# Performance work log

Hardware: AMD Instinct MI355X
Metric: run time of the kernel (lower is better)

The kernel has to match this reference:

```python
import jax, jax.numpy as jnp
import numpy as np

HEADS = 20          # 1280 / 64 head_dim, standard SD UNet attention
LORA_SCALE = 1.0    # lora_scale init arg


def setup_inputs() -> dict:
    key = jax.random.key(0)
    ks = jax.random.split(key, 16)
    def w(k, shape, s=0.02):
        return jax.random.normal(k, shape, dtype=jnp.float32) * s
    H, C, R = 1280, 768, 64  # hidden_size, cross_attention_dim, lora_rank
    return {
        "hidden_states": jax.random.normal(ks[0], (16, 4096, H), dtype=jnp.float32),
        "encoder_hidden_states": jax.random.normal(ks[1], (16, 77, C), dtype=jnp.float32),
        # base attention projections (diffusers: q/k/v no bias, to_out has bias)
        "Wq": w(ks[2], (H, H)), "Wk": w(ks[3], (C, H)), "Wv": w(ks[4], (C, H)),
        "Wo": w(ks[5], (H, H)), "bo": jnp.zeros((H,), dtype=jnp.float32),
        # LoRA adapters (down: in->rank, up: rank->out, no bias)
        "q_down": w(ks[6], (H, R)), "q_up": w(ks[7], (R, H)),
        "k_down": w(ks[8], (C, R)), "k_up": w(ks[9], (R, H)),
        "v_down": w(ks[10], (C, R)), "v_up": w(ks[11], (R, H)),
        "o_down": w(ks[12], (H, R)), "o_up": w(ks[13], (R, H)),
    }


def reference(hidden_states, encoder_hidden_states, Wq, Wk, Wv, Wo, bo,
              q_down, q_up, k_down, k_up, v_down, v_up, o_down, o_up):
    b, sq, _ = hidden_states.shape
    # base projections + LoRA low-rank corrections
    q = hidden_states @ Wq + LORA_SCALE * ((hidden_states @ q_down) @ q_up)
    k = encoder_hidden_states @ Wk + LORA_SCALE * ((encoder_hidden_states @ k_down) @ k_up)
    v = encoder_hidden_states @ Wv + LORA_SCALE * ((encoder_hidden_states @ v_down) @ v_up)

    d = q.shape[-1] // HEADS
    def split_heads(x):  # [b, s, h*d] -> [b, h, s, d]
        return x.reshape(x.shape[0], x.shape[1], HEADS, d).transpose(0, 2, 1, 3)
    qh, kh, vh = split_heads(q), split_heads(k), split_heads(v)

    # scaled dot-product attention (no mask, non-causal, dropout=0)
    scale = 1.0 / np.sqrt(d).astype(np.float32)
    scores = jnp.einsum('bhqd,bhkd->bhqk', qh, kh) * scale
    probs = jax.nn.softmax(scores, axis=-1)
    attn_out = jnp.einsum('bhqk,bhkd->bhqd', probs, vh)
    attn_out = attn_out.transpose(0, 2, 1, 3).reshape(b, sq, HEADS * d)

    # output projection + LoRA on W_O
    out = attn_out @ Wo + bo + LORA_SCALE * ((attn_out @ o_down) @ o_up)
    return out
```

## Files before the change

### kernel.cpp

```cpp
#include <hip/hip_runtime.h>
#include <hip/hip_bf16.h>
#include <stdint.h>

typedef unsigned short u16;
typedef __attribute__((ext_vector_type(8))) short short8;
typedef __attribute__((ext_vector_type(4))) float f32x4;

__device__ __forceinline__ u16 f2bf(float f) {
  union { float f; unsigned u; } v; v.f = f;
  unsigned r = v.u + 0x7fffu + ((v.u >> 16) & 1u);
  return (u16)(r >> 16);
}

__device__ __forceinline__ void g2lds16(const u16* g, u16* l) {
  __builtin_amdgcn_global_load_lds(
      (const __attribute__((address_space(1))) uint32_t*)g,
      (__attribute__((address_space(3))) uint32_t*)l, 16, 0, 0);
}

#define BAR()   asm volatile("s_barrier" ::: "memory")
#define LGKM0() asm volatile("s_waitcnt lgkmcnt(0)" ::: "memory")
#define VM8()   asm volatile("s_waitcnt vmcnt(8)" ::: "memory")
#define VM0()   asm volatile("s_waitcnt vmcnt(0)" ::: "memory")
#define PRIO1() __builtin_amdgcn_s_setprio(1)
#define PRIO0() __builtin_amdgcn_s_setprio(0)

#define QSCALE 0.18033688f

__global__ __launch_bounds__(256) void k_convert(const float* __restrict__ in,
                                                 u16* __restrict__ out, int n8) {
  int i = blockIdx.x * 256 + threadIdx.x;
  if (i >= n8) return;
  const float4* p = (const float4*)(in + (size_t)i * 8);
  float4 a = p[0], b = p[1];
  short8 o;
  o[0] = (short)f2bf(a.x); o[1] = (short)f2bf(a.y);
  o[2] = (short)f2bf(a.z); o[3] = (short)f2bf(a.w);
  o[4] = (short)f2bf(b.x); o[5] = (short)f2bf(b.y);
  o[6] = (short)f2bf(b.z); o[7] = (short)f2bf(b.w);
  *(short8*)(out + (size_t)i * 8) = o;
}

__global__ __launch_bounds__(256) void k_convert_pad(const float* __restrict__ in,
                                                     u16* __restrict__ out,
                                                     int n8_valid, int n8_total) {
  int i = blockIdx.x * 256 + threadIdx.x;
  if (i >= n8_total) return;
  short8 o;
  if (i < n8_valid) {
    const float4* p = (const float4*)(in + (size_t)i * 8);
    float4 a = p[0], b = p[1];
    o[0] = (short)f2bf(a.x); o[1] = (short)f2bf(a.y);
    o[2] = (short)f2bf(a.z); o[3] = (short)f2bf(a.w);
    o[4] = (short)f2bf(b.x); o[5] = (short)f2bf(b.y);
    o[6] = (short)f2bf(b.z); o[7] = (short)f2bf(b.w);
  } else {
#pragma unroll
    for (int e = 0; e < 8; ++e) o[e] = 0;
  }
  *(short8*)(out + (size_t)i * 8) = o;
}

__global__ __launch_bounds__(256) void k_fusew(const float* __restrict__ W,
                                               const float* __restrict__ dn_g,
                                               const float* __restrict__ up_g,
                                               u16* __restrict__ Wt, int K, int N) {
  __shared__ float dn[64][65];
  __shared__ float up[64][17];
  const int k0 = blockIdx.x * 64, n0 = blockIdx.y * 16;
  const int kc = threadIdx.x & 63, ty = threadIdx.x >> 6;
  for (int c = threadIdx.x; c < 4096; c += 256)
    dn[c >> 6][c & 63] = dn_g[(size_t)(k0 + (c >> 6)) * 64 + (c & 63)];
  for (int c = threadIdx.x; c < 1024; c += 256)
    up[c >> 4][c & 15] = up_g[(size_t)(c >> 4) * N + n0 + (c & 15)];
  __syncthreads();
  float acc[4];
#pragma unroll
  for (int e = 0; e < 4; ++e)
    acc[e] = W[(size_t)(k0 + kc) * N + n0 + ty * 4 + e];
#pragma unroll 16
  for (int r = 0; r < 64; ++r) {
    float d = dn[kc][r];
#pragma unroll
    for (int e = 0; e < 4; ++e) acc[e] += d * up[r][ty * 4 + e];
  }
#pragma unroll
  for (int e = 0; e < 4; ++e)
    Wt[(size_t)(n0 + ty * 4 + e) * K + k0 + kc] = f2bf(acc[e]);
}

template <int OUT_MODE>
__global__ __launch_bounds__(256) void k_gemm(const u16* __restrict__ A,
                                              const u16* __restrict__ Bt,
                                              void* __restrict__ Cout,
                                              const float* __restrict__ bias,
                                              int M, int N, int K) {
  __shared__ __align__(16) u16 As[128 * 32];
  __shared__ __align__(16) u16 Bs[128 * 32];
  const int tid = threadIdx.x, lane = tid & 63, w = tid >> 6;
  const int n0 = blockIdx.x * 128, m0 = blockIdx.y * 128;
  const int wm = (w >> 1) * 64, wn = (w & 1) * 64;

  f32x4 acc[4][4];
  f32x4 zf = {0.f, 0.f, 0.f, 0.f};
#pragma unroll
  for (int i = 0; i < 4; ++i)
#pragma unroll
    for (int j = 0; j < 4; ++j) acc[i][j] = zf;

  const int c0 = w, c1 = w + 4;
  const int rA0 = c0 * 16 + (lane >> 2), rA1 = c1 * 16 + (lane >> 2);
  const int kp = (lane & 3) * 8;
  const u16* gA0 = A + (size_t)(m0 + rA0) * K + kp;
  const u16* gA1 = A + (size_t)(m0 + rA1) * K + kp;
  const u16* gB0 = Bt + (size_t)(n0 + rA0) * K + kp;
  const u16* gB1 = Bt + (size_t)(n0 + rA1) * K + kp;
  u16* lA0 = As + c0 * 512;  u16* lA1 = As + c1 * 512;
  u16* lB0 = Bs + c0 * 512;  u16* lB1 = Bs + c1 * 512;

  const int fr = lane & 15, kg = (lane >> 4) * 8;

  for (int k0 = 0; k0 < K; k0 += 32) {
    g2lds16(gA0 + k0, lA0);
    g2lds16(gA1 + k0, lA1);
    g2lds16(gB0 + k0, lB0);
    g2lds16(gB1 + k0, lB1);
    __syncthreads();
    short8 af[4], bf[4];
#pragma unroll
    for (int i = 0; i < 4; ++i)
      af[i] = *(const short8*)(As + (wm + i * 16 + fr) * 32 + kg);
#pragma unroll
    for (int j = 0; j < 4; ++j)
      bf[j] = *(const short8*)(Bs + (wn + j * 16 + fr) * 32 + kg);
#pragma unroll
    for (int i = 0; i < 4; ++i)
#pragma unroll
      for (int j = 0; j < 4; ++j)
        acc[i][j] = __builtin_amdgcn_mfma_f32_16x16x32_bf16(af[i], bf[j], acc[i][j], 0, 0, 0);
    __syncthreads();
  }

  const int rb = (lane >> 4) * 4;
  if (OUT_MODE == 0) {
    u16* C = (u16*)Cout;
#pragma unroll
    for (int i = 0; i < 4; ++i)
#pragma unroll
      for (int j = 0; j < 4; ++j) {
        int col = n0 + wn + j * 16 + fr;
#pragma unroll
        for (int r = 0; r < 4; ++r) {
          int row = m0 + wm + i * 16 + rb + r;
          C[(size_t)row * N + col] = f2bf(acc[i][j][r]);
        }
      }
  } else {
    float* C = (float*)Cout;
#pragma unroll
    for (int i = 0; i < 4; ++i)
#pragma unroll
      for (int j = 0; j < 4; ++j) {
        int col = n0 + wn + j * 16 + fr;
        float bj = bias[col];
#pragma unroll
        for (int r = 0; r < 4; ++r) {
          int row = m0 + wm + i * 16 + rb + r;
          C[(size_t)row * N + col] = acc[i][j][r] + bj;
        }
      }
  }
}


#define GEMM256_TILE_RD()                                                      \
  constexpr int K = 1280;                                                      \
  constexpr int N = 1280;                                                      \
  __shared__ __align__(16) u16 lds[2][2][2][128 * 64];                         \
  const int lane = threadIdx.x & 63, w = threadIdx.x >> 6;                     \
  const int bid = blockIdx.x;                                                  \
  const int tile = (bid & 7) * 160 + (bid >> 3);                               \
  const int n0 = (tile % 5) * 256, m0 = (tile / 5) * 256;                      \
  const int l0 = w * 2;                                                        \
  const int fr = lane & 15;                                                    \
  const int q16b = (lane >> 4) * 16;                                           \
  const int xr = (fr & 7) << 4;                                                \
  const int cT0 = ((0 + q16b) ^ xr) >> 1;                                      \
  const int cT1 = ((64 + q16b) ^ xr) >> 1;                                     \
  const int ha = w >> 2;                                                       \
  const int hb = (w & 3) >> 1;                                                 \
  const int rB0 = (w & 1) * 64;

#define LOAD_AF(P, IB)                                                         \
  do {                                                                         \
    _Pragma("unroll") for (int ii = 0; ii < 4; ++ii) {                         \
      const u16* rp = &lds[P][0][ha][(((IB) + ii) * 16 + fr) * 64];            \
      af[ii][0] = *(const short8*)(rp + cT0);                                  \
      af[ii][1] = *(const short8*)(rp + cT1);                                  \
    }                                                                          \
  } while (0)

#define LOAD_BF(P, JB)                                                         \
  do {                                                                         \
    _Pragma("unroll") for (int jj = 0; jj < 2; ++jj) {                         \
      const u16* rp = &lds[P][1][hb][(rB0 + ((JB) + jj) * 16 + fr) * 64];      \
      bf[(JB) + jj][0] = *(const short8*)(rp + cT0);                           \
      bf[(JB) + jj][1] = *(const short8*)(rp + cT1);                           \
    }                                                                          \
  } while (0)

#define MFMA_Q(IO, JB)                                                         \
  do {                                                                         \
    _Pragma("unroll") for (int t = 0; t < 2; ++t)                              \
        _Pragma("unroll") for (int ii = 0; ii < 4; ++ii)                       \
            _Pragma("unroll") for (int jj = 0; jj < 2; ++jj)                   \
                acc[(IO) + ii][(JB) + jj] =                                    \
        __builtin_amdgcn_mfma_f32_16x16x32_bf16(                               \
            af[ii][t], bf[(JB) + jj][t], acc[(IO) + ii][(JB) + jj], 0, 0, 0);  \
  } while (0)

#define ACC_ZERO()                                                             \
  do {                                                                         \
    f32x4 zf = {0.f, 0.f, 0.f, 0.f};                                           \
    _Pragma("unroll") for (int i = 0; i < 8; ++i)                              \
        _Pragma("unroll") for (int j = 0; j < 4; ++j) acc[i][j] = zf;          \
  } while (0)

template <int OUT_MODE>
__global__ __launch_bounds__(512, 2) void k_gemm256f(const u16* __restrict__ A,
                                                     const u16* __restrict__ Bt,
                                                     void* __restrict__ Cout,
                                                     const float* __restrict__ bias) {
  GEMM256_TILE_RD();
  const u16* gsrc[8];
#pragma unroll
  for (int s = 0; s < 8; ++s) {
    const int side = s >> 2, h = (s >> 1) & 1, l = s & 1;
    const int o = (l0 + l) * 1024 + lane * 16;
    const int row = o >> 7;
    const int scol = (o & 127) ^ ((row & 7) << 4);
    const u16* base = side ? (Bt + (size_t)(n0 + h * 128 + row) * K)
                           : (A + (size_t)(m0 + h * 128 + row) * K);
    gsrc[s] = base + (scol >> 1);
  }

#define STAGE(P, KT)                                                           \
  do {                                                                         \
    _Pragma("unroll") for (int s = 0; s < 8; ++s) {                            \
      const int side = s >> 2, h = (s >> 1) & 1, l = s & 1;                    \
      g2lds16(gsrc[s] + (KT) * 64, &lds[P][side][h][(l0 + l) * 512]);          \
    }                                                                          \
  } while (0)

  short8 af[4][2], bf[4][2];
  f32x4 acc[8][4];
  ACC_ZERO();

  STAGE(0, 0);
  STAGE(1, 1);
  VM8();
  BAR();

  for (int t = 0; t < 20; ++t) {
    const int P = t & 1;
    LOAD_AF(P, 0);
    LOAD_BF(P, 0);
    LOAD_BF(P, 2);
    MFMA_Q(0, 0);
    MFMA_Q(0, 2);
    LOAD_AF(P, 4);
    MFMA_Q(4, 2);
    LGKM0();
    BAR();
    if (t < 18) STAGE(P, t + 2);
    PRIO1(); MFMA_Q(4, 0); PRIO0();
    if (t < 18) { VM8(); } else { VM0(); }
    BAR();
  }
#undef STAGE

  const int rb = (lane >> 4) * 4;
  const int orow = m0 + (w >> 2) * 128;
  const int ocol = n0 + (w & 3) * 64;
  if (OUT_MODE == 0) {
    u16* C = (u16*)Cout;
#pragma unroll
    for (int i = 0; i < 8; ++i)
#pragma unroll
      for (int j = 0; j < 4; ++j) {
        const int col = ocol + j * 16 + fr;
#pragma unroll
        for (int r = 0; r < 4; ++r)
          C[(size_t)(orow + i * 16 + rb + r) * N + col] = f2bf(acc[i][j][r]);
      }
  } else if (OUT_MODE == 1) {
    float* C = (float*)Cout;
#pragma unroll
    for (int i = 0; i < 8; ++i)
#pragma unroll
      for (int j = 0; j < 4; ++j) {
        const int col = ocol + j * 16 + fr;
        const float bj = bias[col];
#pragma unroll
        for (int r = 0; r < 4; ++r)
          C[(size_t)(orow + i * 16 + rb + r) * N + col] = acc[i][j][r] + bj;
      }
  } else {
    u16* C = (u16*)Cout;
#pragma unroll
    for (int i = 0; i < 8; ++i)
#pragma unroll
      for (int j = 0; j < 4; ++j) {
        const int col = ocol + j * 16 + fr;
#pragma unroll
        for (int r = 0; r < 4; ++r)
          C[(size_t)(orow + i * 16 + rb + r) * N + col] = f2bf(acc[i][j][r] * QSCALE);
      }
  }
}

__global__ __launch_bounds__(512) void k_attn(u16* __restrict__ Q,
                                              const u16* __restrict__ Kb,
                                              const u16* __restrict__ Vb) {
  const int mt = blockIdx.x, h = blockIdx.y, b = blockIdx.z;
  const int tid = threadIdx.x, lane = tid & 63, w = tid >> 6;
  const int m0 = b * 4096 + mt * 256;
  const int ccol = h * 64;

  __shared__ __align__(16) u16 Kl[80 * 72];
  __shared__ __align__(16) u16 Vt[64 * 104];
  __shared__ __align__(16) u16 Pl[256 * 104];

  {
    short8 z;
#pragma unroll
    for (int e = 0; e < 8; ++e) z[e] = 0;
    if (tid < 27) ((short8*)Kl)[693 + tid] = z;
    {
      int row = tid >> 1, c0 = 80 + (tid & 1) * 8;
      *(short8*)(Pl + row * 104 + c0) = z;
    }
    for (int c = tid; c < 2048; c += 512)
      Vt[(c >> 5) * 104 + 64 + (c & 31)] = 0;
  }
  __syncthreads();

  for (int c = tid; c < 616; c += 512) {
    int s = c >> 3, d0 = (c & 7) * 8;
    short8 v = *(const short8*)(Kb + (size_t)(b * 77 + s) * 1280 + ccol + d0);
    *(short8*)(Kl + s * 72 + d0) = v;
  }
  for (int c = tid; c < 616; c += 512) {
    int s = c >> 3, d0 = (c & 7) * 8;
    short8 v = *(const short8*)(Vb + (size_t)(b * 77 + s) * 1280 + ccol + d0);
#pragma unroll
    for (int e = 0; e < 8; ++e) Vt[(d0 + e) * 104 + s] = (u16)v[e];
  }

  const int cb = lane & 15, kg = (lane >> 4) * 8;
  short8 qf[2][2];
#pragma unroll
  for (int i = 0; i < 2; ++i)
#pragma unroll
    for (int t = 0; t < 2; ++t) {
      int row = m0 + w * 32 + i * 16 + cb;
      qf[i][t] = *(const short8*)(Q + (size_t)row * 1280 + ccol + t * 32 + kg);
    }
  __syncthreads();

  f32x4 sc[2][5];
  {
    f32x4 zf = {0.f, 0.f, 0.f, 0.f};
#pragma unroll
    for (int i = 0; i < 2; ++i)
#pragma unroll
      for (int j = 0; j < 5; ++j) sc[i][j] = zf;
  }
#pragma unroll
  for (int t = 0; t < 2; ++t) {
    short8 kf[5];
#pragma unroll
    for (int j = 0; j < 5; ++j)
      kf[j] = *(const short8*)(Kl + (j * 16 + cb) * 72 + t * 32 + kg);
#pragma unroll
    for (int i = 0; i < 2; ++i)
#pragma unroll
      for (int j = 0; j < 5; ++j)
        sc[i][j] = __builtin_amdgcn_mfma_f32_16x16x32_bf16(qf[i][t], kf[j], sc[i][j], 0, 0, 0);
  }

  float inv[2][4];
#pragma unroll
  for (int i = 0; i < 2; ++i) {
#pragma unroll
    for (int r = 0; r < 4; ++r) {
      float sum = 0.f;
#pragma unroll
      for (int j = 0; j < 4; ++j) {
        float pv = exp2f(sc[i][j][r]);
        sc[i][j][r] = pv;
        sum += pv;
      }
      {
        float pv = (cb < 13) ? exp2f(sc[i][4][r]) : 0.f;
        sc[i][4][r] = pv;
        sum += pv;
      }
#pragma unroll
      for (int mk = 8; mk >= 1; mk >>= 1) sum += __shfl_xor(sum, mk, 64);
      inv[i][r] = 1.f / sum;
    }
  }

  {
    int rbase = (lane >> 4) * 4;
#pragma unroll
    for (int i = 0; i < 2; ++i)
#pragma unroll
      for (int j = 0; j < 5; ++j)
#pragma unroll
        for (int r = 0; r < 4; ++r)
          Pl[(w * 32 + i * 16 + rbase + r) * 104 + j * 16 + cb] = f2bf(sc[i][j][r]);
  }
  __syncthreads();

  f32x4 o[2][4];
  {
    f32x4 zf = {0.f, 0.f, 0.f, 0.f};
#pragma unroll
    for (int i = 0; i < 2; ++i)
#pragma unroll
      for (int n = 0; n < 4; ++n) o[i][n] = zf;
  }
#pragma unroll
  for (int t = 0; t < 3; ++t) {
    short8 pf[2], vf[4];
#pragma unroll
    for (int i = 0; i < 2; ++i)
      pf[i] = *(const short8*)(Pl + (w * 32 + i * 16 + cb) * 104 + t * 32 + kg);
#pragma unroll
    for (int n = 0; n < 4; ++n)
      vf[n] = *(const short8*)(Vt + (n * 16 + cb) * 104 + t * 32 + kg);
#pragma unroll
    for (int i = 0; i < 2; ++i)
#pragma unroll
      for (int n = 0; n < 4; ++n)
        o[i][n] = __builtin_amdgcn_mfma_f32_16x16x32_bf16(pf[i], vf[n], o[i][n], 0, 0, 0);
  }

  {
    int rbase = (lane >> 4) * 4;
#pragma unroll
    for (int i = 0; i < 2; ++i)
#pragma unroll
      for (int n = 0; n < 4; ++n)
#pragma unroll
        for (int r = 0; r < 4; ++r) {
          int row = m0 + w * 32 + i * 16 + rbase + r;
          Q[(size_t)row * 1280 + ccol + n * 16 + cb] = f2bf(o[i][n][r] * inv[i][r]);
        }
  }
}

extern "C" void kernel_launch(void* const* d_in, const int* in_sizes, int n_in,
                              void* d_out, int out_size, void* d_ws, size_t ws_size,
                              hipStream_t stream) {
  (void)in_sizes; (void)n_in; (void)out_size; (void)ws_size;
  const float* hs  = (const float*)d_in[0];
  const float* ehs = (const float*)d_in[1];
  const float* Wq  = (const float*)d_in[2];
  const float* Wk  = (const float*)d_in[3];
  const float* Wv  = (const float*)d_in[4];
  const float* Wo  = (const float*)d_in[5];
  const float* bo  = (const float*)d_in[6];
  const float* qd  = (const float*)d_in[7];
  const float* qu  = (const float*)d_in[8];
  const float* kd  = (const float*)d_in[9];
  const float* ku  = (const float*)d_in[10];
  const float* vd  = (const float*)d_in[11];
  const float* vu  = (const float*)d_in[12];
  const float* od  = (const float*)d_in[13];
  const float* ou  = (const float*)d_in[14];

  char* p = (char*)d_ws;
  u16* q_buf = (u16*)p;  p += (size_t)65536 * 1280 * 2;
  u16* wq_t  = (u16*)p;  p += (size_t)1280 * 1280 * 2;
  u16* wo_t  = (u16*)p;  p += (size_t)1280 * 1280 * 2;
  u16* wk_t  = (u16*)p;  p += (size_t)1280 * 768 * 2;
  u16* wv_t  = (u16*)p;  p += (size_t)1280 * 768 * 2;
  u16* ehs_b = (u16*)p;  p += (size_t)1280 * 768 * 2;
  u16* k_buf = (u16*)p;  p += (size_t)1280 * 1280 * 2;
  u16* v_buf = (u16*)p;  p += (size_t)1280 * 1280 * 2;
  u16* hs_b  = (u16*)d_out;

  k_convert<<<40960, 256, 0, stream>>>(hs, hs_b, 10485760);
  k_convert_pad<<<480, 256, 0, stream>>>(ehs, ehs_b, 118272, 122880);

  k_fusew<<<dim3(20, 80), 256, 0, stream>>>(Wq, qd, qu, wq_t, 1280, 1280);
  k_fusew<<<dim3(12, 80), 256, 0, stream>>>(Wk, kd, ku, wk_t, 768, 1280);
  k_fusew<<<dim3(12, 80), 256, 0, stream>>>(Wv, vd, vu, wv_t, 768, 1280);
  k_fusew<<<dim3(20, 80), 256, 0, stream>>>(Wo, od, ou, wo_t, 1280, 1280);

  k_gemm256f<2><<<1280, 512, 0, stream>>>(hs_b, wq_t, q_buf, nullptr);
  k_gemm<0><<<dim3(10, 10), 256, 0, stream>>>(ehs_b, wk_t, k_buf, nullptr, 1280, 1280, 768);
  k_gemm<0><<<dim3(10, 10), 256, 0, stream>>>(ehs_b, wv_t, v_buf, nullptr, 1280, 1280, 768);

  k_attn<<<dim3(16, 20, 16), 512, 0, stream>>>(q_buf, k_buf, v_buf);

  k_gemm256f<1><<<1280, 512, 0, stream>>>(q_buf, wo_t, d_out, bo);
}
```

Before: 783.9 us.

## Merge prep kernels, batch K/V GEMMs, restage attention tile through LDS

The ehs pad-convert and the four LoRA weight-fusion launches become one k_prep kernel, and the K and V projections share one launch indexed by blockIdx.z, which removes several small launches. The attention kernel now uses 256-thread blocks covering 128 query rows. Q is loaded into LDS with async global-to-LDS copies and an XOR swizzle, and the output is staged through LDS so it can be written back with coalesced 16-byte stores. Doubling the attention grid gives more blocks per CU but repeats the K/V loads into LDS for each block.

After: 746.7 us. 1.05x faster.

```diff
diff --git a/kernel.cpp b/kernel.cpp
--- a/kernel.cpp
+++ b/kernel.cpp
@@ -41,38 +41,46 @@
   *(short8*)(out + (size_t)i * 8) = o;
 }
 
-__global__ __launch_bounds__(256) void k_convert_pad(const float* __restrict__ in,
-                                                     u16* __restrict__ out,
-                                                     int n8_valid, int n8_total) {
-  int i = blockIdx.x * 256 + threadIdx.x;
-  if (i >= n8_total) return;
-  short8 o;
-  if (i < n8_valid) {
-    const float4* p = (const float4*)(in + (size_t)i * 8);
-    float4 a = p[0], b = p[1];
-    o[0] = (short)f2bf(a.x); o[1] = (short)f2bf(a.y);
-    o[2] = (short)f2bf(a.z); o[3] = (short)f2bf(a.w);
-    o[4] = (short)f2bf(b.x); o[5] = (short)f2bf(b.y);
-    o[6] = (short)f2bf(b.z); o[7] = (short)f2bf(b.w);
-  } else {
-#pragma unroll
-    for (int e = 0; e < 8; ++e) o[e] = 0;
-  }
-  *(short8*)(out + (size_t)i * 8) = o;
-}
-
-__global__ __launch_bounds__(256) void k_fusew(const float* __restrict__ W,
-                                               const float* __restrict__ dn_g,
-                                               const float* __restrict__ up_g,
-                                               u16* __restrict__ Wt, int K, int N) {
+__global__ __launch_bounds__(256) void k_prep(
+    const float* __restrict__ ehs, u16* __restrict__ ehs_b,
+    const float* __restrict__ Wq, const float* __restrict__ qd, const float* __restrict__ qu, u16* __restrict__ wq_t,
+    const float* __restrict__ Wk, const float* __restrict__ kd, const float* __restrict__ ku, u16* __restrict__ wk_t,
+    const float* __restrict__ Wv, const float* __restrict__ vd, const float* __restrict__ vu, u16* __restrict__ wv_t,
+    const float* __restrict__ Wo, const float* __restrict__ od, const float* __restrict__ ou, u16* __restrict__ wo_t) {
   __shared__ float dn[64][65];
   __shared__ float up[64][17];
-  const int k0 = blockIdx.x * 64, n0 = blockIdx.y * 16;
+  int bid = blockIdx.x;
+
+  if (bid < 480) {
+    int i = bid * 256 + threadIdx.x;
+    short8 o;
+    if (i < 118272) {
+      const float4* p = (const float4*)(ehs + (size_t)i * 8);
+      float4 a = p[0], b = p[1];
+      o[0] = (short)f2bf(a.x); o[1] = (short)f2bf(a.y);
+      o[2] = (short)f2bf(a.z); o[3] = (short)f2bf(a.w);
+      o[4] = (short)f2bf(b.x); o[5] = (short)f2bf(b.y);
+      o[6] = (short)f2bf(b.z); o[7] = (short)f2bf(b.w);
+    } else {
+#pragma unroll
+      for (int e = 0; e < 8; ++e) o[e] = 0;
+    }
+    *(short8*)(ehs_b + (size_t)i * 8) = o;
+    return;
+  }
+  bid -= 480;
+  const float *W, *dng, *upg; u16* Wt; int K, bx, by;
+  if (bid < 1600)      { W = Wq; dng = qd; upg = qu; Wt = wq_t; K = 1280; bx = bid % 20; by = bid / 20; }
+  else if (bid < 2560) { bid -= 1600; W = Wk; dng = kd; upg = ku; Wt = wk_t; K = 768;  bx = bid % 12; by = bid / 12; }
+  else if (bid < 3520) { bid -= 2560; W = Wv; dng = vd; upg = vu; Wt = wv_t; K = 768;  bx = bid % 12; by = bid / 12; }
+  else                 { bid -= 3520; W = Wo; dng = od; upg = ou; Wt = wo_t; K = 1280; bx = bid % 20; by = bid / 20; }
+  const int N = 1280;
+  const int k0 = bx * 64, n0 = by * 16;
   const int kc = threadIdx.x & 63, ty = threadIdx.x >> 6;
   for (int c = threadIdx.x; c < 4096; c += 256)
-    dn[c >> 6][c & 63] = dn_g[(size_t)(k0 + (c >> 6)) * 64 + (c & 63)];
+    dn[c >> 6][c & 63] = dng[(size_t)(k0 + (c >> 6)) * 64 + (c & 63)];
   for (int c = threadIdx.x; c < 1024; c += 256)
-    up[c >> 4][c & 15] = up_g[(size_t)(c >> 4) * N + n0 + (c & 15)];
+    up[c >> 4][c & 15] = upg[(size_t)(c >> 4) * N + n0 + (c & 15)];
   __syncthreads();
   float acc[4];
 #pragma unroll
@@ -89,12 +97,14 @@
     Wt[(size_t)(n0 + ty * 4 + e) * K + k0 + kc] = f2bf(acc[e]);
 }
 
-template <int OUT_MODE>
-__global__ __launch_bounds__(256) void k_gemm(const u16* __restrict__ A,
-                                              const u16* __restrict__ Bt,
-                                              void* __restrict__ Cout,
-                                              const float* __restrict__ bias,
-                                              int M, int N, int K) {
+__global__ __launch_bounds__(256) void k_gemmKV(const u16* __restrict__ A,
+                                                const u16* __restrict__ BtK,
+                                                const u16* __restrict__ BtV,
+                                                u16* __restrict__ CK,
+                                                u16* __restrict__ CV) {
+  constexpr int N = 1280, K = 768;
+  const u16* Bt = blockIdx.z ? BtV : BtK;
+  u16* Cout = blockIdx.z ? CV : CK;
   __shared__ __align__(16) u16 As[128 * 32];
   __shared__ __align__(16) u16 Bs[128 * 32];
   const int tid = threadIdx.x, lane = tid & 63, w = tid >> 6;
@@ -142,36 +152,18 @@
   }
 
   const int rb = (lane >> 4) * 4;
-  if (OUT_MODE == 0) {
-    u16* C = (u16*)Cout;
-#pragma unroll
-    for (int i = 0; i < 4; ++i)
-#pragma unroll
-      for (int j = 0; j < 4; ++j) {
-        int col = n0 + wn + j * 16 + fr;
-#pragma unroll
-        for (int r = 0; r < 4; ++r) {
-          int row = m0 + wm + i * 16 + rb + r;
-          C[(size_t)row * N + col] = f2bf(acc[i][j][r]);
-        }
+#pragma unroll
+  for (int i = 0; i < 4; ++i)
+#pragma unroll
+    for (int j = 0; j < 4; ++j) {
+      int col = n0 + wn + j * 16 + fr;
+#pragma unroll
+      for (int r = 0; r < 4; ++r) {
+        int row = m0 + wm + i * 16 + rb + r;
+        Cout[(size_t)row * N + col] = f2bf(acc[i][j][r]);
       }
-  } else {
-    float* C = (float*)Cout;
-#pragma unroll
-    for (int i = 0; i < 4; ++i)
-#pragma unroll
-      for (int j = 0; j < 4; ++j) {
-        int col = n0 + wn + j * 16 + fr;
-        float bj = bias[col];
-#pragma unroll
-        for (int r = 0; r < 4; ++r) {
-          int row = m0 + wm + i * 16 + rb + r;
-          C[(size_t)row * N + col] = acc[i][j][r] + bj;
-        }
-      }
-  }
-}
-
+    }
+}
 
 #define GEMM256_TILE_RD()                                                      \
   constexpr int K = 1280;                                                      \
@@ -282,18 +274,7 @@
   const int rb = (lane >> 4) * 4;
   const int orow = m0 + (w >> 2) * 128;
   const int ocol = n0 + (w & 3) * 64;
-  if (OUT_MODE == 0) {
-    u16* C = (u16*)Cout;
-#pragma unroll
-    for (int i = 0; i < 8; ++i)
-#pragma unroll
-      for (int j = 0; j < 4; ++j) {
-        const int col = ocol + j * 16 + fr;
-#pragma unroll
-        for (int r = 0; r < 4; ++r)
-          C[(size_t)(orow + i * 16 + rb + r) * N + col] = f2bf(acc[i][j][r]);
-      }
-  } else if (OUT_MODE == 1) {
+  if (OUT_MODE == 1) {
     float* C = (float*)Cout;
 #pragma unroll
     for (int i = 0; i < 8; ++i)
@@ -319,54 +300,64 @@
   }
 }
 
-__global__ __launch_bounds__(512) void k_attn(u16* __restrict__ Q,
+__global__ __launch_bounds__(256) void k_attn(u16* __restrict__ Q,
                                               const u16* __restrict__ Kb,
                                               const u16* __restrict__ Vb) {
   const int mt = blockIdx.x, h = blockIdx.y, b = blockIdx.z;
   const int tid = threadIdx.x, lane = tid & 63, w = tid >> 6;
-  const int m0 = b * 4096 + mt * 256;
+  const int m0 = b * 4096 + mt * 128;
   const int ccol = h * 64;
 
+  __shared__ __align__(16) u16 Qs[128 * 64];
   __shared__ __align__(16) u16 Kl[80 * 72];
   __shared__ __align__(16) u16 Vt[64 * 104];
-  __shared__ __align__(16) u16 Pl[256 * 104];
+  __shared__ __align__(16) u16 Pl[128 * 104];
+
+#pragma unroll
+  for (int c = 0; c < 4; ++c) {
+    const int o = (c * 4 + w) * 1024 + lane * 16;
+    const int row = o >> 7;
+    const int scol = (o & 127) ^ ((row & 7) << 4);
+    g2lds16(Q + (size_t)(m0 + row) * 1280 + ccol + (scol >> 1),
+            Qs + (size_t)(c * 4 + w) * 512);
+  }
 
   {
-    short8 z;
-#pragma unroll
-    for (int e = 0; e < 8; ++e) z[e] = 0;
-    if (tid < 27) ((short8*)Kl)[693 + tid] = z;
-    {
-      int row = tid >> 1, c0 = 80 + (tid & 1) * 8;
-      *(short8*)(Pl + row * 104 + c0) = z;
-    }
-    for (int c = tid; c < 2048; c += 512)
+    short8 zz;
+#pragma unroll
+    for (int e = 0; e < 8; ++e) zz[e] = 0;
+    if (tid < 27) ((short8*)Kl)[693 + tid] = zz;
+    { const int prow = tid >> 1, pc0 = 80 + (tid & 1) * 8;
+      *(short8*)(Pl + prow * 104 + pc0) = zz; }
+    for (int c = tid; c < 2048; c += 256)
       Vt[(c >> 5) * 104 + 64 + (c & 31)] = 0;
   }
-  __syncthreads();
-
-  for (int c = tid; c < 616; c += 512) {
+  for (int c = tid; c < 616; c += 256) {
     int s = c >> 3, d0 = (c & 7) * 8;
     short8 v = *(const short8*)(Kb + (size_t)(b * 77 + s) * 1280 + ccol + d0);
     *(short8*)(Kl + s * 72 + d0) = v;
   }
-  for (int c = tid; c < 616; c += 512) {
+  for (int c = tid; c < 616; c += 256) {
     int s = c >> 3, d0 = (c & 7) * 8;
     short8 v = *(const short8*)(Vb + (size_t)(b * 77 + s) * 1280 + ccol + d0);
 #pragma unroll
     for (int e = 0; e < 8; ++e) Vt[(d0 + e) * 104 + s] = (u16)v[e];
   }
-
-  const int cb = lane & 15, kg = (lane >> 4) * 8;
+  __syncthreads();
+
+  const int cb = lane & 15;
+  const int kq = lane >> 4;
+  const int kgu = kq * 8;
+
   short8 qf[2][2];
 #pragma unroll
   for (int i = 0; i < 2; ++i)
 #pragma unroll
-    for (int t = 0; t < 2; ++t) {
-      int row = m0 + w * 32 + i * 16 + cb;
-      qf[i][t] = *(const short8*)(Q + (size_t)row * 1280 + ccol + t * 32 + kg);
+    for (int t2 = 0; t2 < 2; ++t2) {
+      const int r_ = w * 32 + i * 16 + cb;
+      const int bc = (t2 * 64 + kq * 16) ^ ((r_ & 7) << 4);
+      qf[i][t2] = *(const short8*)(Qs + r_ * 64 + (bc >> 1));
     }
-  __syncthreads();
 
   f32x4 sc[2][5];
   {
@@ -377,16 +368,16 @@
       for (int j = 0; j < 5; ++j) sc[i][j] = zf;
   }
 #pragma unroll
-  for (int t = 0; t < 2; ++t) {
+  for (int t2 = 0; t2 < 2; ++t2) {
     short8 kf[5];
 #pragma unroll
     for (int j = 0; j < 5; ++j)
-      kf[j] = *(const short8*)(Kl + (j * 16 + cb) * 72 + t * 32 + kg);
+      kf[j] = *(const short8*)(Kl + (j * 16 + cb) * 72 + t2 * 32 + kgu);
 #pragma unroll
     for (int i = 0; i < 2; ++i)
 #pragma unroll
       for (int j = 0; j < 5; ++j)
-        sc[i][j] = __builtin_amdgcn_mfma_f32_16x16x32_bf16(qf[i][t], kf[j], sc[i][j], 0, 0, 0);
+        sc[i][j] = __builtin_amdgcn_mfma_f32_16x16x32_bf16(qf[i][t2], kf[j], sc[i][j], 0, 0, 0);
   }
 
   float inv[2][4];
@@ -413,7 +404,7 @@
   }
 
   {
-    int rbase = (lane >> 4) * 4;
+    const int rbase = kq * 4;
 #pragma unroll
     for (int i = 0; i < 2; ++i)
 #pragma unroll
@@ -433,14 +424,14 @@
       for (int n = 0; n < 4; ++n) o[i][n] = zf;
   }
 #pragma unroll
-  for (int t = 0; t < 3; ++t) {
+  for (int t2 = 0; t2 < 3; ++t2) {
     short8 pf[2], vf[4];
 #pragma unroll
     for (int i = 0; i < 2; ++i)
-      pf[i] = *(const short8*)(Pl + (w * 32 + i * 16 + cb) * 104 + t * 32 + kg);
+      pf[i] = *(const short8*)(Pl + (w * 32 + i * 16 + cb) * 104 + t2 * 32 + kgu);
 #pragma unroll
     for (int n = 0; n < 4; ++n)
-      vf[n] = *(const short8*)(Vt + (n * 16 + cb) * 104 + t * 32 + kg);
+      vf[n] = *(const short8*)(Vt + (n * 16 + cb) * 104 + t2 * 32 + kgu);
 #pragma unroll
     for (int i = 0; i < 2; ++i)
 #pragma unroll
@@ -449,16 +440,24 @@
   }
 
   {
-    int rbase = (lane >> 4) * 4;
+    const int rbase = kq * 4;
 #pragma unroll
     for (int i = 0; i < 2; ++i)
 #pragma unroll
       for (int n = 0; n < 4; ++n)
 #pragma unroll
-        for (int r = 0; r < 4; ++r) {
-          int row = m0 + w * 32 + i * 16 + rbase + r;
-          Q[(size_t)row * 1280 + ccol + n * 16 + cb] = f2bf(o[i][n][r] * inv[i][r]);
-        }
+        for (int r = 0; r < 4; ++r)
+          Pl[(w * 32 + i * 16 + rbase + r) * 104 + n * 16 + cb] =
+              f2bf(o[i][n][r] * inv[i][r]);
+  }
+  __syncthreads();
+
+#pragma unroll
+  for (int c2 = 0; c2 < 4; ++c2) {
+    const int o2 = (c2 * 256 + tid) * 16;
+    const int row = o2 >> 7, bc = (o2 & 127) >> 1;
+    short8 v = *(const short8*)(Pl + row * 104 + bc);
+    *(short8*)(Q + (size_t)(m0 + row) * 1280 + ccol + bc) = v;
   }
 }
 
@@ -494,18 +493,16 @@
   u16* hs_b  = (u16*)d_out;
 
   k_convert<<<40960, 256, 0, stream>>>(hs, hs_b, 10485760);
-  k_convert_pad<<<480, 256, 0, stream>>>(ehs, ehs_b, 118272, 122880);
-
-  k_fusew<<<dim3(20, 80), 256, 0, stream>>>(Wq, qd, qu, wq_t, 1280, 1280);
-  k_fusew<<<dim3(12, 80), 256, 0, stream>>>(Wk, kd, ku, wk_t, 768, 1280);
-  k_fusew<<<dim3(12, 80), 256, 0, stream>>>(Wv, vd, vu, wv_t, 768, 1280);
-  k_fusew<<<dim3(20, 80), 256, 0, stream>>>(Wo, od, ou, wo_t, 1280, 1280);
+  k_prep<<<5600, 256, 0, stream>>>(ehs, ehs_b,
+                                   Wq, qd, qu, wq_t,
+                                   Wk, kd, ku, wk_t,
+                                   Wv, vd, vu, wv_t,
+                                   Wo, od, ou, wo_t);
 
   k_gemm256f<2><<<1280, 512, 0, stream>>>(hs_b, wq_t, q_buf, nullptr);
-  k_gemm<0><<<dim3(10, 10), 256, 0, stream>>>(ehs_b, wk_t, k_buf, nullptr, 1280, 1280, 768);
-  k_gemm<0><<<dim3(10, 10), 256, 0, stream>>>(ehs_b, wv_t, v_buf, nullptr, 1280, 1280, 768);
-
-  k_attn<<<dim3(16, 20, 16), 512, 0, stream>>>(q_buf, k_buf, v_buf);
+  k_gemmKV<<<dim3(10, 10, 2), 256, 0, stream>>>(ehs_b, wk_t, wv_t, k_buf, v_buf);
+
+  k_attn<<<dim3(32, 20, 16), 256, 0, stream>>>(q_buf, k_buf, v_buf);
 
   k_gemm256f<1><<<1280, 512, 0, stream>>>(q_buf, wo_t, d_out, bo);
 }
```
